# Kernel optimization log

Measured on AMD Instinct MI355X. Metric: run time of the kernel, lower is better.

Reference implementation:

```python
import jax, jax.numpy as jnp
import numpy as np

EPS = 1e-4  # SPDRectified clamp epsilon (standard spdnet default)


def _rect(m):
    # ReEig: eigendecompose, clamp eigenvalues at EPS, reconstruct
    w, v = jnp.linalg.eigh(m)
    w = jnp.maximum(w, EPS)
    return jnp.einsum('...ij,...j,...kj->...ik', v, w, v)


def _trans(m, W):
    # SPDTransform (BiMap): W^T X W, W has orthonormal columns (Stiefel)
    return jnp.einsum('ij,...ik,kl->...jl', W, m, W)


def setup_inputs():
    key = jax.random.key(0)
    ks = jax.random.split(key, 8)
    B, T, n, hs = 128, 64, 57, 2
    A = jax.random.normal(ks[0], (B, T, n, n), jnp.float32)
    # SPD inputs: covariance-like matrices
    x = jnp.einsum('btij,btkj->btik', A, A) / n + 0.1 * jnp.eye(n, dtype=jnp.float32)
    W1 = jnp.linalg.qr(jax.random.normal(ks[1], (n, 20), jnp.float32))[0]
    W2 = jnp.linalg.qr(jax.random.normal(ks[2], (20, 10), jnp.float32))[0]
    W3 = jnp.linalg.qr(jax.random.normal(ks[3], (10, hs), jnp.float32))[0]
    d = hs * (hs + 1) // 2
    lin_w = jax.random.normal(ks[4], (17, d), jnp.float32) * 0.1
    lin_b = jax.random.normal(ks[5], (17,), jnp.float32) * 0.1
    alpha = jax.random.normal(ks[6], (1,), jnp.float32)
    return {"x": x, "W1": W1, "W2": W2, "W3": W3,
            "lin_w": lin_w, "lin_b": lin_b, "alpha": alpha}


def reference(x, W1, W2, W3, lin_w, lin_b, alpha):
    B, T, n, _ = x.shape
    hs = W3.shape[1]
    # input_layer is independent of the recurrence -> vectorize over B*T
    z = x.reshape(B * T, n, n)
    z = _rect(_trans(z, W1))   # (B*T, 20, 20)
    z = _rect(_trans(z, W2))   # (B*T, 10, 10)
    z = _rect(_trans(z, W3))   # (B*T, hs, hs)
    a = z.reshape(B, T, hs, hs).transpose(1, 0, 2, 3)  # (T, B, hs, hs)

    s = jax.nn.sigmoid(alpha[0])
    iu = jnp.triu_indices(hs)  # SPDVectorize: upper-triangular entries

    def step(h, a_t):
        h_new = s * a_t + (1.0 - s) * _rect(h)
        # SPDTangentSpace: matrix log via eigh, then vectorize upper triangle
        w, v = jnp.linalg.eigh(h_new)
        logm = jnp.einsum('bij,bj,bkj->bik', v, jnp.log(w), v)
        vec = logm[:, iu[0], iu[1]]          # (B, hs*(hs+1)/2)
        out = vec @ lin_w.T + lin_b          # (B, 17)
        return h_new, out

    h0 = jnp.zeros((B, hs, hs), x.dtype)
    _, outs = jax.lax.scan(step, h0, a)      # outs: (T, B, 17)
    return outs.transpose(1, 0, 2)           # (B, T, 17)
```

## Files before the change

kernel.cpp:

```cpp
#include <hip/hip_runtime.h>
#include <math.h>

#define BB    128
#define TT    64
#define NSZ   57
#define NN    3249
#define MTOT  8192
#define NOUT  17
#define RECT_EPS 1e-4f

#define WC_OFF   0
#define C00_OFF  128
#define C01_OFF  (128 + 3264)
#define C11_OFF  (128 + 2*3264)
#define A00_OFF  (128 + 3*3264)
#define A01_OFF  (A00_OFF + MTOT)
#define A11_OFF  (A01_OFF + MTOT)

__global__ __launch_bounds__(256) void prep_kernel(
    const float* __restrict__ W1, const float* __restrict__ W2,
    const float* __restrict__ W3, float* __restrict__ ws)
{
    __shared__ float W12[57 * 10];
    __shared__ float WcS[57 * 2];
    const int tid = threadIdx.x;

    for (int i = tid; i < 57 * 10; i += 256) {
        int p = i / 10, j = i % 10;
        float s = 0.f;
        #pragma unroll
        for (int k = 0; k < 20; ++k) s = fmaf(W1[p * 20 + k], W2[k * 10 + j], s);
        W12[i] = s;
    }
    __syncthreads();
    for (int i = tid; i < 57 * 2; i += 256) {
        int p = i / 2, j = i % 2;
        float s = 0.f;
        #pragma unroll
        for (int k = 0; k < 10; ++k) s = fmaf(W12[p * 10 + k], W3[k * 2 + j], s);
        WcS[i] = s;
        ws[WC_OFF + i] = s;
    }
    __syncthreads();
    float* c00 = ws + C00_OFF;
    float* c01 = ws + C01_OFF;
    float* c11 = ws + C11_OFF;
    for (int f = tid; f < NN; f += 256) {
        int p = f / 57, q = f % 57;
        float p0 = WcS[p * 2], p1 = WcS[p * 2 + 1];
        float q0 = WcS[q * 2], q1 = WcS[q * 2 + 1];
        c00[f] = p0 * q0;
        c01[f] = p0 * q1;
        c11[f] = p1 * q1;
    }
}

#define PROJ_GRID 1024
__global__ __launch_bounds__(256) void proj_kernel(
    const float* __restrict__ x, float* __restrict__ ws)
{
    const float* __restrict__ c00 = ws + C00_OFF;
    const float* __restrict__ c01 = ws + C01_OFF;
    const float* __restrict__ c11 = ws + C11_OFF;

    const int tid = threadIdx.x;

    float k00[13], k01[13], k11[13];
    #pragma unroll
    for (int i = 0; i < 13; ++i) {
        int f = tid + 256 * i;
        if (f < NN) { k00[i] = c00[f]; k01[i] = c01[f]; k11[i] = c11[f]; }
        else        { k00[i] = 0.f;    k01[i] = 0.f;    k11[i] = 0.f;    }
    }

    const int m0 = blockIdx.x * 8;
    const float* __restrict__ xb = x + (size_t)m0 * NN;

    float a0[8], a1[8], a2[8];
    #pragma unroll
    for (int j = 0; j < 8; ++j) { a0[j] = 0.f; a1[j] = 0.f; a2[j] = 0.f; }

    #pragma unroll
    for (int i = 0; i < 12; ++i) {
        const int f = tid + 256 * i;
        #pragma unroll
        for (int j = 0; j < 8; ++j) {
            float xv = xb[(size_t)j * NN + f];
            a0[j] = fmaf(k00[i], xv, a0[j]);
            a1[j] = fmaf(k01[i], xv, a1[j]);
            a2[j] = fmaf(k11[i], xv, a2[j]);
        }
    }
    if (tid < NN - 3072) {
        const int f = tid + 3072;
        #pragma unroll
        for (int j = 0; j < 8; ++j) {
            float xv = xb[(size_t)j * NN + f];
            a0[j] = fmaf(k00[12], xv, a0[j]);
            a1[j] = fmaf(k01[12], xv, a1[j]);
            a2[j] = fmaf(k11[12], xv, a2[j]);
        }
    }

    #pragma unroll
    for (int j = 0; j < 8; ++j) {
        #pragma unroll
        for (int off = 32; off > 0; off >>= 1) {
            a0[j] += __shfl_down(a0[j], off);
            a1[j] += __shfl_down(a1[j], off);
            a2[j] += __shfl_down(a2[j], off);
        }
    }

    __shared__ float red[4][24];
    const int lane = tid & 63, wv = tid >> 6;
    if (lane == 0) {
        #pragma unroll
        for (int j = 0; j < 8; ++j) {
            red[wv][j * 3 + 0] = a0[j];
            red[wv][j * 3 + 1] = a1[j];
            red[wv][j * 3 + 2] = a2[j];
        }
    }
    __syncthreads();
    if (tid < 24) {
        float s = red[0][tid] + red[1][tid] + red[2][tid] + red[3][tid];
        int j = tid / 3, c = tid % 3;
        ws[A00_OFF + c * MTOT + m0 + j] = s;
    }
}

__global__ __launch_bounds__(64) void scan_kernel(
    const float* __restrict__ ws, const float* __restrict__ lin_w,
    const float* __restrict__ lin_b, const float* __restrict__ alpha,
    float* __restrict__ out)
{
    const int b = blockIdx.x;
    const int lane = threadIdx.x;
    const float* a00 = ws + A00_OFF;
    const float* a01 = ws + A01_OFF;
    const float* a11 = ws + A11_OFF;

    const float s  = 1.f / (1.f + expf(-alpha[0]));
    const float os = 1.f - s;

    float lw0 = 0.f, lw1 = 0.f, lw2 = 0.f, lb = 0.f;
    if (lane < NOUT) {
        lw0 = lin_w[lane * 3 + 0];
        lw1 = lin_w[lane * 3 + 1];
        lw2 = lin_w[lane * 3 + 2];
        lb  = lin_b[lane];
    }

    const int mbase = b * TT;
    float pa00 = a00[mbase + lane];
    float pa01 = a01[mbase + lane];
    float pa11 = a11[mbase + lane];

    float r00 = RECT_EPS, r01 = 0.f, r11 = RECT_EPS;

    for (int t = 0; t < TT; ++t) {
        float at00 = __shfl(pa00, t);
        float at01 = __shfl(pa01, t);
        float at11 = __shfl(pa11, t);

        float h00 = fmaf(s, at00, os * r00);
        float h01 = fmaf(s, at01, os * r01);
        float h11 = fmaf(s, at11, os * r11);

        float mm = 0.5f * (h00 + h11);
        float dd = 0.5f * (h00 - h11);
        float rr = sqrtf(fmaf(dd, dd, h01 * h01));
        float l1 = mm + rr, l2 = mm - rr;

        float lg1 = logf(l1), lg2 = logf(l2);
        float pp = 0.5f * (lg1 + lg2);
        float qq = (rr > 1e-20f) ? (lg1 - lg2) / (2.f * rr) : 0.f;
        float L00 = pp + qq * dd;
        float L01 = qq * h01;
        float L11 = pp - qq * dd;

        if (lane < NOUT) {
            float v = fmaf(L00, lw0, fmaf(L01, lw1, fmaf(L11, lw2, lb)));
            out[(size_t)(mbase + t) * NOUT + lane] = v;
        }

        float c1 = fmaxf(l1, RECT_EPS), c2 = fmaxf(l2, RECT_EPS);
        float k1 = 0.5f * (c1 + c2);
        float k2 = (rr > 1e-20f) ? (c1 - c2) / (2.f * rr) : 0.f;
        r00 = fmaf(k2, dd, k1);
        r01 = k2 * h01;
        r11 = fmaf(-k2, dd, k1);
    }
}

extern "C" void kernel_launch(void* const* d_in, const int* in_sizes, int n_in,
                              void* d_out, int out_size, void* d_ws, size_t ws_size,
                              hipStream_t stream) {
    const float* x     = (const float*)d_in[0];
    const float* W1    = (const float*)d_in[1];
    const float* W2    = (const float*)d_in[2];
    const float* W3    = (const float*)d_in[3];
    const float* lin_w = (const float*)d_in[4];
    const float* lin_b = (const float*)d_in[5];
    const float* alpha = (const float*)d_in[6];
    float* out = (float*)d_out;
    float* ws  = (float*)d_ws;

    prep_kernel<<<1, 256, 0, stream>>>(W1, W2, W3, ws);
    proj_kernel<<<PROJ_GRID, 256, 0, stream>>>(x, ws);
    scan_kernel<<<BB, 64, 0, stream>>>(ws, lin_w, lin_b, alpha, out);
}
```

Measured before the change: 191.6 us.

## Vectorize projection loads with float4 via residue-grouped rows and LDS-staged coefficients

The projection kernel now groups matrices by row index modulo 4, so each row's start, shifted back by that residue, is 16-byte aligned. That allows float4 loads of x. The coefficient vectors are staged once per block into shared memory, shifted and zero-padded to match the alignment, so the few neighbouring-row elements pulled in by the wider loads are multiplied by zero. This targets the scalar-load and latency bottleneck of streaming the large input. In exchange it adds an LDS fill and sync per block, shared-memory reads of the coefficients, and a 4-blocks-per-CU launch bound.

```diff
diff --git a/kernel.cpp b/kernel.cpp
--- a/kernel.cpp
+++ b/kernel.cpp
@@ -56,49 +56,59 @@
 }
 
 #define PROJ_GRID 1024
-__global__ __launch_bounds__(256) void proj_kernel(
+__global__ __launch_bounds__(256, 4) void proj_kernel(
     const float* __restrict__ x, float* __restrict__ ws)
 {
-    const float* __restrict__ c00 = ws + C00_OFF;
-    const float* __restrict__ c01 = ws + C01_OFF;
-    const float* __restrict__ c11 = ws + C11_OFF;
+    __shared__ __align__(16) float cS[3][3264];
+    __shared__ float red[4][24];
 
     const int tid = threadIdx.x;
-
-    float k00[13], k01[13], k11[13];
-    #pragma unroll
-    for (int i = 0; i < 13; ++i) {
-        int f = tid + 256 * i;
-        if (f < NN) { k00[i] = c00[f]; k01[i] = c01[f]; k11[i] = c11[f]; }
-        else        { k00[i] = 0.f;    k01[i] = 0.f;    k11[i] = 0.f;    }
-    }
-
-    const int m0 = blockIdx.x * 8;
-    const float* __restrict__ xb = x + (size_t)m0 * NN;
+    const int r   = blockIdx.x & 3;
+    const int idx = blockIdx.x >> 2;
+
+    {
+        const float* __restrict__ c00 = ws + C00_OFF;
+        const float* __restrict__ c01 = ws + C01_OFF;
+        const float* __restrict__ c11 = ws + C11_OFF;
+        for (int k = tid; k < 3252; k += 256) {
+            int f = k - r;
+            bool ok = (f >= 0) && (f < NN);
+            cS[0][k] = ok ? c00[f] : 0.f;
+            cS[1][k] = ok ? c01[f] : 0.f;
+            cS[2][k] = ok ? c11[f] : 0.f;
+        }
+    }
+    __syncthreads();
+
+    const float4* __restrict__ cv0 = (const float4*)&cS[0][0];
+    const float4* __restrict__ cv1 = (const float4*)&cS[1][0];
+    const float4* __restrict__ cv2 = (const float4*)&cS[2][0];
 
     float a0[8], a1[8], a2[8];
     #pragma unroll
     for (int j = 0; j < 8; ++j) { a0[j] = 0.f; a1[j] = 0.f; a2[j] = 0.f; }
 
     #pragma unroll
-    for (int i = 0; i < 12; ++i) {
-        const int f = tid + 256 * i;
-        #pragma unroll
-        for (int j = 0; j < 8; ++j) {
-            float xv = xb[(size_t)j * NN + f];
-            a0[j] = fmaf(k00[i], xv, a0[j]);
-            a1[j] = fmaf(k01[i], xv, a1[j]);
-            a2[j] = fmaf(k11[i], xv, a2[j]);
-        }
-    }
-    if (tid < NN - 3072) {
-        const int f = tid + 3072;
-        #pragma unroll
-        for (int j = 0; j < 8; ++j) {
-            float xv = xb[(size_t)j * NN + f];
-            a0[j] = fmaf(k00[12], xv, a0[j]);
-            a1[j] = fmaf(k01[12], xv, a1[j]);
-            a2[j] = fmaf(k11[12], xv, a2[j]);
+    for (int kk = 0; kk < 8; ++kk) {
+        const int m = r + 4 * (idx + 256 * kk);
+        const float4* __restrict__ xv4 = (const float4*)(x + (size_t)m * NN - r);
+
+        #pragma unroll
+        for (int i = 0; i < 3; ++i) {
+            const int v = tid + 256 * i;
+            float4 xv = xv4[v];
+            float4 c0 = cv0[v], c1 = cv1[v], c2 = cv2[v];
+            a0[kk] = fmaf(c0.x, xv.x, fmaf(c0.y, xv.y, fmaf(c0.z, xv.z, fmaf(c0.w, xv.w, a0[kk]))));
+            a1[kk] = fmaf(c1.x, xv.x, fmaf(c1.y, xv.y, fmaf(c1.z, xv.z, fmaf(c1.w, xv.w, a1[kk]))));
+            a2[kk] = fmaf(c2.x, xv.x, fmaf(c2.y, xv.y, fmaf(c2.z, xv.z, fmaf(c2.w, xv.w, a2[kk]))));
+        }
+        if (tid < 813 - 768) {
+            const int v = tid + 768;
+            float4 xv = xv4[v];
+            float4 c0 = cv0[v], c1 = cv1[v], c2 = cv2[v];
+            a0[kk] = fmaf(c0.x, xv.x, fmaf(c0.y, xv.y, fmaf(c0.z, xv.z, fmaf(c0.w, xv.w, a0[kk]))));
+            a1[kk] = fmaf(c1.x, xv.x, fmaf(c1.y, xv.y, fmaf(c1.z, xv.z, fmaf(c1.w, xv.w, a1[kk]))));
+            a2[kk] = fmaf(c2.x, xv.x, fmaf(c2.y, xv.y, fmaf(c2.z, xv.z, fmaf(c2.w, xv.w, a2[kk]))));
         }
     }
 
@@ -111,8 +121,6 @@
             a2[j] += __shfl_down(a2[j], off);
         }
     }
-
-    __shared__ float red[4][24];
     const int lane = tid & 63, wv = tid >> 6;
     if (lane == 0) {
         #pragma unroll
@@ -126,7 +134,8 @@
     if (tid < 24) {
         float s = red[0][tid] + red[1][tid] + red[2][tid] + red[3][tid];
         int j = tid / 3, c = tid % 3;
-        ws[A00_OFF + c * MTOT + m0 + j] = s;
+        int m = r + 4 * (idx + 256 * j);
+        ws[A00_OFF + c * MTOT + m] = s;
     }
 }
 
```

Result: no change. 193.5 us (+1.0%).
